# Optimization experiments

Hardware: AMD Instinct MI355X
Metric: run time of the kernel (lower is better)

Reference implementation:

```python
import jax, jax.numpy as jnp
import numpy as np

B = 524288
HID = 128
EPS = 1e-3

def _linear_params(key, fan_in, fan_out):
    k1, k2 = jax.random.split(key)
    s = 1.0 / np.sqrt(fan_in)
    W = jax.random.uniform(k1, (fan_out, fan_in), jnp.float32, -s, s)
    b = jax.random.uniform(k2, (fan_out,), jnp.float32, -s, s)
    return W, b

def _mlp(x, W1, b1, W2, b2):
    # Linear -> Tanh -> Linear (torch weight layout [out,in])
    h = jnp.tanh(x @ W1.T + b1)
    return h @ W2.T + b2

def setup_inputs() -> dict:
    key = jax.random.key(0)
    ks = jax.random.split(key, 12)
    q = jax.random.normal(ks[0], (B, 2), jnp.float32)
    qd = jax.random.normal(ks[1], (B, 2), jnp.float32)
    u = jax.random.normal(ks[2], (B, 2), jnp.float32)
    Wm1, bm1 = _linear_params(ks[3], 2, HID)
    Wm2, bm2 = _linear_params(ks[4], HID, 4)
    Wc1, bc1 = _linear_params(ks[5], 4, HID)
    Wc2, bc2 = _linear_params(ks[6], HID, 4)
    Wg1, bg1 = _linear_params(ks[7], 2, HID)
    Wg2, bg2 = _linear_params(ks[8], HID, 2)
    Wt1, bt1 = _linear_params(ks[9], 6, HID)
    Wt2, bt2 = _linear_params(ks[10], HID, 2)
    return dict(q=q, qd=qd, u=u,
                Wm1=Wm1, bm1=bm1, Wm2=Wm2, bm2=bm2,
                Wc1=Wc1, bc1=bc1, Wc2=Wc2, bc2=bc2,
                Wg1=Wg1, bg1=bg1, Wg2=Wg2, bg2=bg2,
                Wt1=Wt1, bt1=bt1, Wt2=Wt2, bt2=bt2)

def reference(q, qd, u,
              Wm1, bm1, Wm2, bm2,
              Wc1, bc1, Wc2, bc2,
              Wg1, bg1, Wg2, bg2,
              Wt1, bt1, Wt2, bt2):
    b = q.shape[0]
    # SPD mass matrix: M = tril(L) tril(L)^T + eps*I, L from MLP(q)
    L = _mlp(q, Wm1, bm1, Wm2, bm2).reshape(b, 2, 2)
    L = jnp.tril(L)
    I = jnp.eye(2, dtype=q.dtype)
    M = jnp.einsum('bik,bjk->bij', L, L) + EPS * I
    # Coriolis matrix from [q, qd]
    C = _mlp(jnp.concatenate([q, qd], axis=-1), Wc1, bc1, Wc2, bc2).reshape(b, 2, 2)
    # Gravity vector from q
    g = _mlp(q, Wg1, bg1, Wg2, bg2)
    # Non-conservative torque from [q, qd, u]
    tau_nc = _mlp(jnp.concatenate([q, qd, u], axis=-1), Wt1, bt1, Wt2, bt2)
    rhs = u - jnp.einsum('bij,bj->bi', C, qd) - g - tau_nc
    qdd = jnp.linalg.solve(M, rhs[..., None])[..., 0]
    return (qdd, M, C, g, tau_nc)
```

## Files before the change

### kernel.cpp

```cpp
#include <hip/hip_runtime.h>

#define HID 128
#define EPSM 1e-3f

__global__ void phynn_pack(const float* __restrict__ Wm1, const float* __restrict__ bm1,
                           const float* __restrict__ Wm2, const float* __restrict__ bm2,
                           const float* __restrict__ Wc1, const float* __restrict__ bc1,
                           const float* __restrict__ Wc2, const float* __restrict__ bc2,
                           const float* __restrict__ Wg1, const float* __restrict__ bg1,
                           const float* __restrict__ Wg2, const float* __restrict__ bg2,
                           const float* __restrict__ Wt1, const float* __restrict__ bt1,
                           const float* __restrict__ Wt2, const float* __restrict__ bt2,
                           float* __restrict__ P)
{
    int i = threadIdx.x;
    if (i < HID) {
        float* p = P + i * 32;
        p[0]  = Wm1[2*i];     p[1]  = Wm1[2*i+1];  p[2]  = bm1[i];      p[3]  = Wm2[i];
        p[4]  = Wm2[128+i];   p[5]  = Wm2[256+i];  p[6]  = Wm2[384+i];  p[7]  = Wg1[2*i];
        p[8]  = Wg1[2*i+1];   p[9]  = bg1[i];      p[10] = Wg2[i];      p[11] = Wg2[128+i];
        p[12] = Wc1[4*i];     p[13] = Wc1[4*i+1];  p[14] = Wc1[4*i+2];  p[15] = Wc1[4*i+3];
        p[16] = bc1[i];       p[17] = Wc2[i];      p[18] = Wc2[128+i];  p[19] = Wc2[256+i];
        p[20] = Wc2[384+i];   p[21] = Wt1[6*i];    p[22] = Wt1[6*i+1];  p[23] = Wt1[6*i+2];
        p[24] = Wt1[6*i+3];   p[25] = Wt1[6*i+4];  p[26] = Wt1[6*i+5];  p[27] = bt1[i];
        p[28] = Wt2[i];       p[29] = Wt2[128+i];  p[30] = 0.f;         p[31] = 0.f;
    }
    if (i == HID) {
        float* t = P + 4096;
        t[0] = bm2[0]; t[1] = bm2[1]; t[2]  = bm2[2]; t[3]  = bm2[3];
        t[4] = bc2[0]; t[5] = bc2[1]; t[6]  = bc2[2]; t[7]  = bc2[3];
        t[8] = bg2[0]; t[9] = bg2[1]; t[10] = bt2[0]; t[11] = bt2[1];
    }
}

__device__ __forceinline__ float fast_tanh(float x)
{
    float e = __expf(2.0f * x);
    float r = __builtin_amdgcn_rcpf(e + 1.0f);
    return __builtin_fmaf(-2.0f, r, 1.0f);
}

#define NPE 2

__global__ __launch_bounds__(256, 4) void phynn_main(
    const float2* __restrict__ q, const float2* __restrict__ qd, const float2* __restrict__ u,
    const float* __restrict__ P, float* __restrict__ out, int B)
{
    __shared__ float4 W[1024 + 3];

    const float4* Pv = (const float4*)P;
    #pragma unroll
    for (int k = 0; k < 4; ++k) W[threadIdx.x + 256 * k] = Pv[threadIdx.x + 256 * k];
    if (threadIdx.x < 3) W[1024 + threadIdx.x] = Pv[1024 + threadIdx.x];
    __syncthreads();

    const int half = B >> 1;
    const int tid  = blockIdx.x * 256 + threadIdx.x;
    if (tid >= half) return;

    int e[NPE];
    e[0] = tid;
    e[1] = tid + half;

    float q0[NPE], q1[NPE], d0[NPE], d1[NPE], u0[NPE], u1[NPE];
    #pragma unroll
    for (int s = 0; s < NPE; ++s) {
        float2 vq = q[e[s]];  q0[s] = vq.x; q1[s] = vq.y;
        float2 vd = qd[e[s]]; d0[s] = vd.x; d1[s] = vd.y;
        float2 vu = u[e[s]];  u0[s] = vu.x; u1[s] = vu.y;
    }

    float aL0[NPE] = {}, aL2[NPE] = {}, aL3[NPE] = {};
    float aC0[NPE] = {}, aC1[NPE] = {}, aC2[NPE] = {}, aC3[NPE] = {};
    float aG0[NPE] = {}, aG1[NPE] = {};
    float aT0[NPE] = {}, aT1[NPE] = {};

    #pragma unroll 2
    for (int i = 0; i < HID; ++i) {
        const float4 v0 = W[i*8+0];
        const float4 v1 = W[i*8+1];
        const float4 v2 = W[i*8+2];
        const float4 v3 = W[i*8+3];
        const float4 v4 = W[i*8+4];
        const float4 v5 = W[i*8+5];
        const float4 v6 = W[i*8+6];
        const float4 v7 = W[i*8+7];
        #pragma unroll
        for (int s = 0; s < NPE; ++s) {
            float am = fmaf(v0.x, q0[s], fmaf(v0.y, q1[s], v0.z));
            float hm = fast_tanh(am);
            aL0[s] = fmaf(v0.w, hm, aL0[s]);
            aL2[s] = fmaf(v1.y, hm, aL2[s]);
            aL3[s] = fmaf(v1.z, hm, aL3[s]);
            float ag = fmaf(v1.w, q0[s], fmaf(v2.x, q1[s], v2.y));
            float hg = fast_tanh(ag);
            aG0[s] = fmaf(v2.z, hg, aG0[s]);
            aG1[s] = fmaf(v2.w, hg, aG1[s]);
            float ac = fmaf(v3.x, q0[s], fmaf(v3.y, q1[s],
                       fmaf(v3.z, d0[s], fmaf(v3.w, d1[s], v4.x))));
            float hc = fast_tanh(ac);
            aC0[s] = fmaf(v4.y, hc, aC0[s]);
            aC1[s] = fmaf(v4.z, hc, aC1[s]);
            aC2[s] = fmaf(v4.w, hc, aC2[s]);
            aC3[s] = fmaf(v5.x, hc, aC3[s]);
            float at = fmaf(v5.y, q0[s], fmaf(v5.z, q1[s],
                       fmaf(v5.w, d0[s], fmaf(v6.x, d1[s],
                       fmaf(v6.y, u0[s], fmaf(v6.z, u1[s], v6.w))))));
            float ht = fast_tanh(at);
            aT0[s] = fmaf(v7.x, ht, aT0[s]);
            aT1[s] = fmaf(v7.y, ht, aT1[s]);
        }
    }

    const float4 bm2v = W[1024];
    const float4 bc2v = W[1025];
    const float4 bgt  = W[1026];

    float*  outf = out;
    float2* o_qdd = (float2*)outf;
    float4* o_M   = (float4*)(outf + (size_t)2 * B);
    float4* o_C   = (float4*)(outf + (size_t)6 * B);
    float2* o_g   = (float2*)(outf + (size_t)10 * B);
    float2* o_t   = (float2*)(outf + (size_t)12 * B);

    #pragma unroll
    for (int s = 0; s < NPE; ++s) {
        float l00 = aL0[s] + bm2v.x;
        float l10 = aL2[s] + bm2v.z;
        float l11 = aL3[s] + bm2v.w;
        float M00 = fmaf(l00, l00, EPSM);
        float M01 = l00 * l10;
        float M11 = fmaf(l10, l10, fmaf(l11, l11, EPSM));

        float C00 = aC0[s] + bc2v.x;
        float C01 = aC1[s] + bc2v.y;
        float C10 = aC2[s] + bc2v.z;
        float C11 = aC3[s] + bc2v.w;

        float g0 = aG0[s] + bgt.x;
        float g1 = aG1[s] + bgt.y;
        float t0 = aT0[s] + bgt.z;
        float t1 = aT1[s] + bgt.w;

        float rhs0 = u0[s] - fmaf(C00, d0[s], C01 * d1[s]) - g0 - t0;
        float rhs1 = u1[s] - fmaf(C10, d0[s], C11 * d1[s]) - g1 - t1;

        float det  = fmaf(M00, M11, -(M01 * M01));
        float qdd0 = fmaf(M11, rhs0, -(M01 * rhs1)) / det;
        float qdd1 = fmaf(M00, rhs1, -(M01 * rhs0)) / det;

        o_qdd[e[s]] = make_float2(qdd0, qdd1);
        o_M[e[s]]   = make_float4(M00, M01, M01, M11);
        o_C[e[s]]   = make_float4(C00, C01, C10, C11);
        o_g[e[s]]   = make_float2(g0, g1);
        o_t[e[s]]   = make_float2(t0, t1);
    }
}

extern "C" void kernel_launch(void* const* d_in, const int* in_sizes, int n_in,
                              void* d_out, int out_size, void* d_ws, size_t ws_size,
                              hipStream_t stream)
{
    const float* q   = (const float*)d_in[0];
    const float* qd  = (const float*)d_in[1];
    const float* u   = (const float*)d_in[2];
    const float* Wm1 = (const float*)d_in[3];
    const float* bm1 = (const float*)d_in[4];
    const float* Wm2 = (const float*)d_in[5];
    const float* bm2 = (const float*)d_in[6];
    const float* Wc1 = (const float*)d_in[7];
    const float* bc1 = (const float*)d_in[8];
    const float* Wc2 = (const float*)d_in[9];
    const float* bc2 = (const float*)d_in[10];
    const float* Wg1 = (const float*)d_in[11];
    const float* bg1 = (const float*)d_in[12];
    const float* Wg2 = (const float*)d_in[13];
    const float* bg2 = (const float*)d_in[14];
    const float* Wt1 = (const float*)d_in[15];
    const float* bt1 = (const float*)d_in[16];
    const float* Wt2 = (const float*)d_in[17];
    const float* bt2 = (const float*)d_in[18];

    const int B = in_sizes[0] / 2;
    float* P = (float*)d_ws;

    hipLaunchKernelGGL(phynn_pack, dim3(1), dim3(192), 0, stream,
                       Wm1, bm1, Wm2, bm2, Wc1, bc1, Wc2, bc2,
                       Wg1, bg1, Wg2, bg2, Wt1, bt1, Wt2, bt2, P);

    const int half   = B / 2;
    const int blocks = (half + 255) / 256;
    hipLaunchKernelGGL(phynn_main, dim3(blocks), dim3(256), 0, stream,
                       (const float2*)q, (const float2*)qd, (const float2*)u,
                       P, (float*)d_out, B);
}
```

Measured before the change: 110.9 us.

## Use packed fp16 dot2 for gravity, Coriolis and torque MLPs with prescaled exp2 tanh

```diff
diff --git a/kernel.cpp b/kernel.cpp
--- a/kernel.cpp
+++ b/kernel.cpp
@@ -2,6 +2,50 @@
 
 #define HID 128
 #define EPSM 1e-3f
+#define KLOG2E 2.8853900817779268f
+
+typedef __fp16 h2 __attribute__((ext_vector_type(2)));
+
+__device__ __forceinline__ h2 as_h2(float f){ union U{float f; h2 h;} u; u.f = f; return u.h; }
+__device__ __forceinline__ float h2_bits(h2 h){ union U{h2 h; float f;} u; u.h = h; return u.f; }
+
+__device__ __forceinline__ float fdot2f(h2 a, h2 b, float c){
+#if __has_builtin(__builtin_amdgcn_fdot2)
+    return __builtin_amdgcn_fdot2(a, b, c, false);
+#else
+    return fmaf((float)a.x, (float)b.x, fmaf((float)a.y, (float)b.y, c));
+#endif
+}
+__device__ __forceinline__ h2 pkrtz(float a, float b){
+#if __has_builtin(__builtin_amdgcn_cvt_pkrtz)
+    return __builtin_amdgcn_cvt_pkrtz(a, b);
+#else
+    h2 r; r.x = (__fp16)a; r.y = (__fp16)b; return r;
+#endif
+}
+__device__ __forceinline__ float aexp2(float x){
+#if __has_builtin(__builtin_amdgcn_exp2f)
+    return __builtin_amdgcn_exp2f(x);
+#else
+    return __expf(0.6931471805599453f * x);
+#endif
+}
+__device__ __forceinline__ float arcp(float x){
+#if __has_builtin(__builtin_amdgcn_rcpf)
+    return __builtin_amdgcn_rcpf(x);
+#else
+    return 1.0f / x;
+#endif
+}
+__device__ __forceinline__ float tanh_s(float a){
+    float t = aexp2(a);
+    float r = arcp(t + 1.0f);
+    return fmaf(-2.0f, r, 1.0f);
+}
+
+__device__ __forceinline__ float h2f(float a, float b){
+    h2 h; h.x = (__fp16)a; h.y = (__fp16)b; return h2_bits(h);
+}
 
 __global__ void phynn_pack(const float* __restrict__ Wm1, const float* __restrict__ bm1,
                            const float* __restrict__ Wm2, const float* __restrict__ bm2,
@@ -13,31 +57,46 @@
                            const float* __restrict__ Wt2, const float* __restrict__ bt2,
                            float* __restrict__ P)
 {
-    int i = threadIdx.x;
-    if (i < HID) {
-        float* p = P + i * 32;
-        p[0]  = Wm1[2*i];     p[1]  = Wm1[2*i+1];  p[2]  = bm1[i];      p[3]  = Wm2[i];
-        p[4]  = Wm2[128+i];   p[5]  = Wm2[256+i];  p[6]  = Wm2[384+i];  p[7]  = Wg1[2*i];
-        p[8]  = Wg1[2*i+1];   p[9]  = bg1[i];      p[10] = Wg2[i];      p[11] = Wg2[128+i];
-        p[12] = Wc1[4*i];     p[13] = Wc1[4*i+1];  p[14] = Wc1[4*i+2];  p[15] = Wc1[4*i+3];
-        p[16] = bc1[i];       p[17] = Wc2[i];      p[18] = Wc2[128+i];  p[19] = Wc2[256+i];
-        p[20] = Wc2[384+i];   p[21] = Wt1[6*i];    p[22] = Wt1[6*i+1];  p[23] = Wt1[6*i+2];
-        p[24] = Wt1[6*i+3];   p[25] = Wt1[6*i+4];  p[26] = Wt1[6*i+5];  p[27] = bt1[i];
-        p[28] = Wt2[i];       p[29] = Wt2[128+i];  p[30] = 0.f;         p[31] = 0.f;
-    }
-    if (i == HID) {
-        float* t = P + 4096;
+    const float k = KLOG2E;
+    int p = threadIdx.x;
+    if (p < 64) {
+        int n0 = 2*p, n1 = 2*p + 1;
+        float* o = P + p * 40;
+        o[0]  = k*Wm1[2*n0];   o[1]  = k*Wm1[2*n0+1]; o[2]  = k*bm1[n0];     o[3]  = Wm2[n0];
+        o[4]  = Wm2[256+n0];   o[5]  = Wm2[384+n0];   o[6]  = k*Wm1[2*n1];   o[7]  = k*Wm1[2*n1+1];
+        o[8]  = k*bm1[n1];     o[9]  = Wm2[n1];       o[10] = Wm2[256+n1];   o[11] = Wm2[384+n1];
+        o[12] = h2f(k*Wg1[2*n0], k*Wg1[2*n0+1]);
+        o[13] = h2f(k*Wg1[2*n1], k*Wg1[2*n1+1]);
+        o[14] = k*bg1[n0];     o[15] = k*bg1[n1];
+        o[16] = h2f(Wg2[n0],      Wg2[n1]);
+        o[17] = h2f(Wg2[128+n0],  Wg2[128+n1]);
+        o[18] = h2f(k*Wc1[4*n0],   k*Wc1[4*n0+1]);
+        o[19] = h2f(k*Wc1[4*n0+2], k*Wc1[4*n0+3]);
+        o[20] = h2f(k*Wc1[4*n1],   k*Wc1[4*n1+1]);
+        o[21] = h2f(k*Wc1[4*n1+2], k*Wc1[4*n1+3]);
+        o[22] = k*bc1[n0];     o[23] = k*bc1[n1];
+        o[24] = h2f(Wc2[n0],      Wc2[n1]);
+        o[25] = h2f(Wc2[128+n0],  Wc2[128+n1]);
+        o[26] = h2f(Wc2[256+n0],  Wc2[256+n1]);
+        o[27] = h2f(Wc2[384+n0],  Wc2[384+n1]);
+        o[28] = h2f(k*Wt1[6*n0],   k*Wt1[6*n0+1]);
+        o[29] = h2f(k*Wt1[6*n0+2], k*Wt1[6*n0+3]);
+        o[30] = h2f(k*Wt1[6*n0+4], k*Wt1[6*n0+5]);
+        o[31] = k*bt1[n0];
+        o[32] = h2f(k*Wt1[6*n1],   k*Wt1[6*n1+1]);
+        o[33] = h2f(k*Wt1[6*n1+2], k*Wt1[6*n1+3]);
+        o[34] = h2f(k*Wt1[6*n1+4], k*Wt1[6*n1+5]);
+        o[35] = k*bt1[n1];
+        o[36] = h2f(Wt2[n0],     Wt2[n1]);
+        o[37] = h2f(Wt2[128+n0], Wt2[128+n1]);
+        o[38] = 0.f; o[39] = 0.f;
+    }
+    if (p == 64) {
+        float* t = P + 2560;
         t[0] = bm2[0]; t[1] = bm2[1]; t[2]  = bm2[2]; t[3]  = bm2[3];
         t[4] = bc2[0]; t[5] = bc2[1]; t[6]  = bc2[2]; t[7]  = bc2[3];
         t[8] = bg2[0]; t[9] = bg2[1]; t[10] = bt2[0]; t[11] = bt2[1];
     }
-}
-
-__device__ __forceinline__ float fast_tanh(float x)
-{
-    float e = __expf(2.0f * x);
-    float r = __builtin_amdgcn_rcpf(e + 1.0f);
-    return __builtin_fmaf(-2.0f, r, 1.0f);
 }
 
 #define NPE 2
@@ -46,12 +105,9 @@
     const float2* __restrict__ q, const float2* __restrict__ qd, const float2* __restrict__ u,
     const float* __restrict__ P, float* __restrict__ out, int B)
 {
-    __shared__ float4 W[1024 + 3];
-
+    __shared__ float4 Ws[640 + 3];
     const float4* Pv = (const float4*)P;
-    #pragma unroll
-    for (int k = 0; k < 4; ++k) W[threadIdx.x + 256 * k] = Pv[threadIdx.x + 256 * k];
-    if (threadIdx.x < 3) W[1024 + threadIdx.x] = Pv[1024 + threadIdx.x];
+    for (int t = threadIdx.x; t < 643; t += 256) Ws[t] = Pv[t];
     __syncthreads();
 
     const int half = B >> 1;
@@ -63,11 +119,15 @@
     e[1] = tid + half;
 
     float q0[NPE], q1[NPE], d0[NPE], d1[NPE], u0[NPE], u1[NPE];
+    h2 qh[NPE], dh[NPE], uh[NPE];
     #pragma unroll
     for (int s = 0; s < NPE; ++s) {
         float2 vq = q[e[s]];  q0[s] = vq.x; q1[s] = vq.y;
         float2 vd = qd[e[s]]; d0[s] = vd.x; d1[s] = vd.y;
         float2 vu = u[e[s]];  u0[s] = vu.x; u1[s] = vu.y;
+        qh[s] = pkrtz(q0[s], q1[s]);
+        dh[s] = pkrtz(d0[s], d1[s]);
+        uh[s] = pkrtz(u0[s], u1[s]);
     }
 
     float aL0[NPE] = {}, aL2[NPE] = {}, aL3[NPE] = {};
@@ -76,47 +136,61 @@
     float aT0[NPE] = {}, aT1[NPE] = {};
 
     #pragma unroll 2
-    for (int i = 0; i < HID; ++i) {
-        const float4 v0 = W[i*8+0];
-        const float4 v1 = W[i*8+1];
-        const float4 v2 = W[i*8+2];
-        const float4 v3 = W[i*8+3];
-        const float4 v4 = W[i*8+4];
-        const float4 v5 = W[i*8+5];
-        const float4 v6 = W[i*8+6];
-        const float4 v7 = W[i*8+7];
+    for (int p = 0; p < 64; ++p) {
+        const float4 v0 = Ws[p*10+0];
+        const float4 v1 = Ws[p*10+1];
+        const float4 v2 = Ws[p*10+2];
+        const float4 v3 = Ws[p*10+3];
+        const float4 v4 = Ws[p*10+4];
+        const float4 v5 = Ws[p*10+5];
+        const float4 v6 = Ws[p*10+6];
+        const float4 v7 = Ws[p*10+7];
+        const float4 v8 = Ws[p*10+8];
+        const float4 v9 = Ws[p*10+9];
+
+        const h2 gw0 = as_h2(v3.x), gw1 = as_h2(v3.y);
+        const h2 gl0 = as_h2(v4.x), gl1 = as_h2(v4.y);
+        const h2 c0a = as_h2(v4.z), c0b = as_h2(v4.w);
+        const h2 c1a = as_h2(v5.x), c1b = as_h2(v5.y);
+        const h2 cl0 = as_h2(v6.x), cl1 = as_h2(v6.y), cl2 = as_h2(v6.z), cl3 = as_h2(v6.w);
+        const h2 t0a = as_h2(v7.x), t0b = as_h2(v7.y), t0c = as_h2(v7.z);
+        const h2 t1a = as_h2(v8.x), t1b = as_h2(v8.y), t1c = as_h2(v8.z);
+        const h2 tl0 = as_h2(v9.x), tl1 = as_h2(v9.y);
+
         #pragma unroll
         for (int s = 0; s < NPE; ++s) {
-            float am = fmaf(v0.x, q0[s], fmaf(v0.y, q1[s], v0.z));
-            float hm = fast_tanh(am);
-            aL0[s] = fmaf(v0.w, hm, aL0[s]);
-            aL2[s] = fmaf(v1.y, hm, aL2[s]);
-            aL3[s] = fmaf(v1.z, hm, aL3[s]);
-            float ag = fmaf(v1.w, q0[s], fmaf(v2.x, q1[s], v2.y));
-            float hg = fast_tanh(ag);
-            aG0[s] = fmaf(v2.z, hg, aG0[s]);
-            aG1[s] = fmaf(v2.w, hg, aG1[s]);
-            float ac = fmaf(v3.x, q0[s], fmaf(v3.y, q1[s],
-                       fmaf(v3.z, d0[s], fmaf(v3.w, d1[s], v4.x))));
-            float hc = fast_tanh(ac);
-            aC0[s] = fmaf(v4.y, hc, aC0[s]);
-            aC1[s] = fmaf(v4.z, hc, aC1[s]);
-            aC2[s] = fmaf(v4.w, hc, aC2[s]);
-            aC3[s] = fmaf(v5.x, hc, aC3[s]);
-            float at = fmaf(v5.y, q0[s], fmaf(v5.z, q1[s],
-                       fmaf(v5.w, d0[s], fmaf(v6.x, d1[s],
-                       fmaf(v6.y, u0[s], fmaf(v6.z, u1[s], v6.w))))));
-            float ht = fast_tanh(at);
-            aT0[s] = fmaf(v7.x, ht, aT0[s]);
-            aT1[s] = fmaf(v7.y, ht, aT1[s]);
+            float am0 = fmaf(v0.x, q0[s], fmaf(v0.y, q1[s], v0.z));
+            float am1 = fmaf(v1.z, q0[s], fmaf(v1.w, q1[s], v2.x));
+            float hm0 = tanh_s(am0);
+            float hm1 = tanh_s(am1);
+            aL0[s] = fmaf(v0.w, hm0, fmaf(v2.y, hm1, aL0[s]));
+            aL2[s] = fmaf(v1.x, hm0, fmaf(v2.z, hm1, aL2[s]));
+            aL3[s] = fmaf(v1.y, hm0, fmaf(v2.w, hm1, aL3[s]));
+            float ag0 = fdot2f(gw0, qh[s], v3.z);
+            float ag1 = fdot2f(gw1, qh[s], v3.w);
+            h2 hg = pkrtz(tanh_s(ag0), tanh_s(ag1));
+            aG0[s] = fdot2f(gl0, hg, aG0[s]);
+            aG1[s] = fdot2f(gl1, hg, aG1[s]);
+            float ac0 = fdot2f(c0a, qh[s], fdot2f(c0b, dh[s], v5.z));
+            float ac1 = fdot2f(c1a, qh[s], fdot2f(c1b, dh[s], v5.w));
+            h2 hc = pkrtz(tanh_s(ac0), tanh_s(ac1));
+            aC0[s] = fdot2f(cl0, hc, aC0[s]);
+            aC1[s] = fdot2f(cl1, hc, aC1[s]);
+            aC2[s] = fdot2f(cl2, hc, aC2[s]);
+            aC3[s] = fdot2f(cl3, hc, aC3[s]);
+            float at0 = fdot2f(t0a, qh[s], fdot2f(t0b, dh[s], fdot2f(t0c, uh[s], v7.w)));
+            float at1 = fdot2f(t1a, qh[s], fdot2f(t1b, dh[s], fdot2f(t1c, uh[s], v8.w)));
+            h2 ht = pkrtz(tanh_s(at0), tanh_s(at1));
+            aT0[s] = fdot2f(tl0, ht, aT0[s]);
+            aT1[s] = fdot2f(tl1, ht, aT1[s]);
         }
     }
 
-    const float4 bm2v = W[1024];
-    const float4 bc2v = W[1025];
-    const float4 bgt  = W[1026];
-
-    float*  outf = out;
+    const float4 bm2v = Ws[640];
+    const float4 bc2v = Ws[641];
+    const float4 bgt  = Ws[642];
+
+    float*  outf  = out;
     float2* o_qdd = (float2*)outf;
     float4* o_M   = (float4*)(outf + (size_t)2 * B);
     float4* o_C   = (float4*)(outf + (size_t)6 * B);
@@ -145,9 +219,11 @@
         float rhs0 = u0[s] - fmaf(C00, d0[s], C01 * d1[s]) - g0 - t0;
         float rhs1 = u1[s] - fmaf(C10, d0[s], C11 * d1[s]) - g1 - t1;
 
-        float det  = fmaf(M00, M11, -(M01 * M01));
-        float qdd0 = fmaf(M11, rhs0, -(M01 * rhs1)) / det;
-        float qdd1 = fmaf(M00, rhs1, -(M01 * rhs0)) / det;
+        float det = fmaf(M00, M11, -(M01 * M01));
+        float r0  = arcp(det);
+        float rdet = r0 * fmaf(-det, r0, 2.0f);
+        float qdd0 = fmaf(M11, rhs0, -(M01 * rhs1)) * rdet;
+        float qdd1 = fmaf(M00, rhs1, -(M01 * rhs0)) * rdet;
 
         o_qdd[e[s]] = make_float2(qdd0, qdd1);
         o_M[e[s]]   = make_float4(M00, M01, M01, M11);
@@ -184,7 +260,7 @@
     const int B = in_sizes[0] / 2;
     float* P = (float*)d_ws;
 
-    hipLaunchKernelGGL(phynn_pack, dim3(1), dim3(192), 0, stream,
+    hipLaunchKernelGGL(phynn_pack, dim3(1), dim3(128), 0, stream,
                        Wm1, bm1, Wm2, bm2, Wc1, bc1, Wc2, bc2,
                        Wg1, bg1, Wg2, bg2, Wt1, bt1, Wt2, bt2, P);
 
```

New measurement: 90.18 us. 1.23x faster.
